# Kernel optimization log

Measured on AMD Instinct MI355X. Metric: run time of the kernel, lower is better.

## Reference

```python
import jax, jax.numpy as jnp
import numpy as np

N, D, E = 16384, 2048, 64   # tokens, d_model, num_experts
K = 9                        # self.k = min(k+1, num_experts) with k=8
EPS = 0.01
SIGMA = 1.0 / E              # Normal(0, 1/num_experts) stddev


def setup_inputs() -> dict:
    key = jax.random.key(0)
    ks = jax.random.split(key, 6)
    x = jax.random.normal(ks[0], (N, D), jnp.float32)
    Wr = jax.random.normal(ks[1], (D, E), jnp.float32) * 0.02
    br = jnp.zeros((E,), jnp.float32)
    Wn = jax.random.normal(ks[2], (D, E), jnp.float32) * 0.02
    bn = jnp.zeros((E,), jnp.float32)
    noise_eps = jax.random.normal(ks[3], (N, E), jnp.float32)
    # torch: (-empty.exponential_()).log() -> log of Exp(1) samples
    gumbel_noise = jnp.log(jax.random.exponential(ks[4], (N, E), jnp.float32))
    return {"x": x, "Wr": Wr, "br": br, "Wn": Wn, "bn": bn,
            "noise_eps": noise_eps, "gumbel_noise": gumbel_noise}


def reference(x, Wr, br, Wn, bn, noise_eps, gumbel_noise):
    raw_logits = x @ Wr + br                              # [N, E]
    noise_stddev = jax.nn.softplus(x @ Wn + bn) + EPS     # [N, E]
    noisy_logits = raw_logits + noise_eps * noise_stddev  # [N, E]

    top_vals, top_idx = jax.lax.top_k(noisy_logits, K)    # [N, K] sorted desc
    # scatter ones at top-k indices (indices unique per row)
    hard_mask = jax.nn.one_hot(top_idx, E, dtype=noisy_logits.dtype).sum(axis=1)  # [N, E]

    # gumbel-softmax straight-through relaxation
    mask_soft = jax.nn.softmax(noisy_logits + gumbel_noise, axis=-1)
    expert_mask = hard_mask - jax.lax.stop_gradient(mask_soft) + mask_soft

    route_prob = jax.nn.softmax(noisy_logits, axis=-1)    # [N, E]
    importance = jax.nn.softmax(raw_logits, axis=-1).sum(axis=0)  # [E]

    # load: P(raw + noise > threshold), Normal(0, 1/E) CDF per original
    threshold = top_vals[:, K - 1]                        # [N]
    z = (threshold[:, None] - raw_logits) / noise_stddev  # [N, E]
    cdf = 0.5 * (1.0 + jax.scipy.special.erf(z / (SIGMA * jnp.sqrt(jnp.float32(2.0)))))
    load = (1.0 - cdf).sum(axis=0)                        # [E]

    return (expert_mask, route_prob, importance, load)
```

## Files before the change

kernel.cpp:

```cpp
#include <hip/hip_runtime.h>
#include <hip/hip_bf16.h>
#include <math.h>

#define N_TOK 16384
#define DIM   2048
#define NE    64
#define TOPK  9

#define ROWS     64
#define DC       64
#define NCHUNK   (DIM / DC)
#define NTHREADS 512

typedef short  short8  __attribute__((ext_vector_type(8)));
typedef float  float4_ __attribute__((ext_vector_type(4)));
typedef unsigned short ushort_t;

__device__ __forceinline__ unsigned pk2(float a, float b) {
    float2 f; f.x = a; f.y = b;
    __hip_bfloat162 h = __float22bfloat162_rn(f);
    unsigned u;
    __builtin_memcpy(&u, &h, 4);
    return u;
}

__device__ __forceinline__ void cvt8(const float4_ va, const float4_ vb,
                                     short8* h, short8* l) {
    union { short8 s; unsigned u[4]; } H, L;
    const float f[8] = {va[0], va[1], va[2], va[3], vb[0], vb[1], vb[2], vb[3]};
#pragma unroll
    for (int i = 0; i < 4; ++i) {
        const float a = f[2 * i], b = f[2 * i + 1];
        const unsigned p = pk2(a, b);
        H.u[i] = p;
        const float ha = __uint_as_float(p << 16);
        const float hb = __uint_as_float(p & 0xffff0000u);
        L.u[i] = pk2(a - ha, b - hb);
    }
    *h = H.s; *l = L.s;
}

__device__ __forceinline__ void wave_max64_2(float& a, float& b) {
#pragma unroll
    for (int off = 32; off > 0; off >>= 1) {
        const float ax = __shfl_xor(a, off, 64);
        const float bx = __shfl_xor(b, off, 64);
        a = fmaxf(a, ax);
        b = fmaxf(b, bx);
    }
}

__device__ __forceinline__ void wave_sum64_3(float& a, float& b, float& c) {
#pragma unroll
    for (int off = 32; off > 0; off >>= 1) {
        const float ax = __shfl_xor(a, off, 64);
        const float bx = __shfl_xor(b, off, 64);
        const float cx = __shfl_xor(c, off, 64);
        a += ax;
        b += bx;
        c += cx;
    }
}

__global__ __launch_bounds__(256)
void prep_w(const float* __restrict__ Wr, const float* __restrict__ Wn,
            ushort_t* __restrict__ wsW)
{
    const int gid = blockIdx.x * 256 + threadIdx.x;
    const int l   = gid & 63;
    const int ct  = (gid >> 6) & 7;
    const int kcg = gid >> 9;
    const int n   = ct * 16 + (l & 15);
    const int k0  = kcg * 32 + (l >> 4) * 8;
    const float* src = (n < NE) ? (Wr + n) : (Wn + (n - NE));
    union { short8 s; ushort_t us[8]; } H, L;
#pragma unroll
    for (int j = 0; j < 8; ++j) {
        const float v = src[(size_t)(k0 + j) * NE];
        const unsigned uv = __float_as_uint(v);
        const unsigned hb = (uv + 0x7fffu + ((uv >> 16) & 1u)) & 0xffff0000u;
        const float lo = v - __uint_as_float(hb);
        const unsigned ul = __float_as_uint(lo);
        H.us[j] = (ushort_t)(hb >> 16);
        L.us[j] = (ushort_t)((ul + 0x7fffu + ((ul >> 16) & 1u)) >> 16);
    }
    const size_t s0 = (size_t)(kcg * 8 + ct) * 2;
    *(short8*)(wsW + s0 * 512 + l * 8)         = H.s;
    *(short8*)(wsW + (s0 + 1) * 512 + l * 8)   = L.s;
}

__global__ __launch_bounds__(NTHREADS, 2)
void moe_main(const float* __restrict__ x,
              const float* __restrict__ br,
              const float* __restrict__ bn,
              const float* __restrict__ noise_eps,
              const float* __restrict__ gumbel,
              const ushort_t* __restrict__ wsW,
              float* __restrict__ out)
{
    __shared__ __align__(16) float smem[8320];

    const int t    = threadIdx.x;
    const int lane = t & 63;
    const int w    = t >> 6;
    const int c4   = lane & 15;
    const int q    = lane >> 4;
    const int rg   = w >> 2;
    const int cg   = w & 3;
    const int row0 = blockIdx.x * ROWS;

    const float* pA[2];
#pragma unroll
    for (int rt = 0; rt < 2; ++rt)
        pA[rt] = x + (size_t)(row0 + (2 * rg + rt) * 16 + c4) * DIM + q * 8;

    float4_ acc[2][2];
#pragma unroll
    for (int rt = 0; rt < 2; ++rt)
#pragma unroll
        for (int cc = 0; cc < 2; ++cc)
            acc[rt][cc] = (float4_)(0.f);

    const char* wsB = (const char*)wsW;

#pragma unroll 2
    for (int ch = 0; ch < NCHUNK; ++ch) {
        short8 bh[2][2], bl[2][2];
#pragma unroll
        for (int kc = 0; kc < 2; ++kc)
#pragma unroll
            for (int cc = 0; cc < 2; ++cc) {
                const int ct = 2 * cg + cc;
                const size_t off = (size_t)(((ch * 2 + kc) * 8) + ct) * 2048
                                 + (size_t)lane * 16;
                bh[kc][cc] = *(const short8*)(wsB + off);
                bl[kc][cc] = *(const short8*)(wsB + off + 1024);
            }
#pragma unroll
        for (int kc = 0; kc < 2; ++kc)
#pragma unroll
            for (int rt = 0; rt < 2; ++rt) {
                const float4_ va = *(const float4_*)(pA[rt] + ch * DC + kc * 32);
                const float4_ vb = *(const float4_*)(pA[rt] + ch * DC + kc * 32 + 4);
                short8 ah, al;
                cvt8(va, vb, &ah, &al);
#pragma unroll
                for (int cc = 0; cc < 2; ++cc) {
                    acc[rt][cc] = __builtin_amdgcn_mfma_f32_16x16x32_bf16(ah, bh[kc][cc], acc[rt][cc], 0, 0, 0);
                    acc[rt][cc] = __builtin_amdgcn_mfma_f32_16x16x32_bf16(al, bh[kc][cc], acc[rt][cc], 0, 0, 0);
                    acc[rt][cc] = __builtin_amdgcn_mfma_f32_16x16x32_bf16(ah, bl[kc][cc], acc[rt][cc], 0, 0, 0);
                }
            }
    }

    float* rawS = &smem[0];
    float* noiS = &smem[4160];
#pragma unroll
    for (int rt = 0; rt < 2; ++rt)
#pragma unroll
        for (int cc = 0; cc < 2; ++cc) {
            const int colg = (2 * cg + cc) * 16 + c4;
            float* basep = (colg < NE) ? rawS : noiS;
            const int col = colg & 63;
#pragma unroll
            for (int v = 0; v < 4; ++v) {
                const int row = (2 * rg + rt) * 16 + q * 4 + v;
                basep[row * 65 + col] = acc[rt][cc][v];
            }
        }
    __syncthreads();

    const float br_l = br[lane];
    const float bn_l = bn[lane];

    float epsv[8], gumv[8];
#pragma unroll
    for (int r = 0; r < 8; ++r) {
        const int row = row0 + w * 8 + r;
        epsv[r] = noise_eps[(size_t)row * NE + lane];
        gumv[r] = gumbel  [(size_t)row * NE + lane];
    }

    float imp_acc = 0.f, load_acc = 0.f;
    float* out_em   = out;
    float* out_rp   = out + (size_t)N_TOK * NE;
    float* out_imp  = out + (size_t)2 * N_TOK * NE;
    float* out_load = out_imp + NE;

#pragma unroll 1
    for (int r = 0; r < 8; ++r) {
        const int lrow = w * 8 + r;
        const int row  = row0 + lrow;
        const float raw = rawS[lrow * 65 + lane] + br_l;
        const float nl  = noiS[lrow * 65 + lane] + bn_l;
        const float sd = fmaxf(nl, 0.f) + log1pf(expf(-fabsf(nl))) + 0.01f;
        const float noisy = fmaf(epsv[r], sd, raw);

        const unsigned uk  = __float_as_uint(noisy);
        const unsigned key = uk ^ ((uk & 0x80000000u) ? 0xFFFFFFFFu : 0x80000000u);
        unsigned res = 0;
#pragma unroll
        for (int bit = 31; bit >= 0; --bit) {
            const unsigned cand = res | (1u << bit);
            const int cnt = __popcll(__ballot(key >= cand));
            if (cnt >= TOPK) res = cand;
        }
        const float thr  = __uint_as_float(res ^ ((res & 0x80000000u) ? 0x80000000u : 0xFFFFFFFFu));
        const float hard = (key >= res) ? 1.f : 0.f;

        const float g = noisy + gumv[r];
        float mg = g, mr = raw;
        wave_max64_2(mg, mr);

        const float eg = expf(g - mg);
        const float en = expf(noisy - thr);
        const float er = expf(raw - mr);
        float sg = eg, sn = en, sr = er;
        wave_sum64_3(sg, sn, sr);

        const float ms = eg / sg;
        const float em = (hard - ms) + ms;
        const float rp = en / sn;
        imp_acc += er / sr;

        const float z = (thr - raw) / sd;
        load_acc += 0.5f * erfcf(z * 45.254833995939045f);

        out_em[(size_t)row * NE + lane] = em;
        out_rp[(size_t)row * NE + lane] = rp;
    }

    __syncthreads();
    smem[w * 64 + lane]       = imp_acc;
    smem[512 + w * 64 + lane] = load_acc;
    __syncthreads();
    if (w == 0) {
        float s1 = 0.f, s2 = 0.f;
#pragma unroll
        for (int i = 0; i < 8; ++i) {
            s1 += smem[i * 64 + lane];
            s2 += smem[512 + i * 64 + lane];
        }
        atomicAdd(&out_imp[lane], s1);
        atomicAdd(&out_load[lane], s2);
    }
}

extern "C" void kernel_launch(void* const* d_in, const int* in_sizes, int n_in,
                              void* d_out, int out_size, void* d_ws, size_t ws_size,
                              hipStream_t stream)
{
    const float* x         = (const float*)d_in[0];
    const float* Wr        = (const float*)d_in[1];
    const float* br        = (const float*)d_in[2];
    const float* Wn        = (const float*)d_in[3];
    const float* bn        = (const float*)d_in[4];
    const float* noise_eps = (const float*)d_in[5];
    const float* gumbel    = (const float*)d_in[6];
    float* out = (float*)d_out;
    ushort_t* wsW = (ushort_t*)d_ws;

    (void)hipMemsetAsync((char*)d_out + (size_t)2 * N_TOK * NE * sizeof(float), 0,
                         2 * NE * sizeof(float), stream);
    prep_w<<<128, 256, 0, stream>>>(Wr, Wn, wsW);
    moe_main<<<N_TOK / ROWS, NTHREADS, 0, stream>>>(
        x, br, bn, noise_eps, gumbel, wsW, out);
}
```

Measured before the change: 278.4 us.

## Stage x tiles into LDS with async loads and split K across wave halves

Each block now handles 32 rows instead of 64. The two halves of the waves each reduce half of the d_model dimension, and their partial results are summed through shared memory in the epilogue. Activation tiles are fetched with global_load_lds into a 4-deep XOR-swizzled LDS ring buffer, while weight fragments are double-buffered in registers. Manual vmcnt waits and barriers overlap these loads with the MFMA work. The aim is to hide global-load latency and raise occupancy (launch bounds go from 2 to 4 blocks), at the cost of hand-tuned wait counts that are fragile and an extra reduction step.

```diff
diff --git a/kernel.cpp b/kernel.cpp
--- a/kernel.cpp
+++ b/kernel.cpp
@@ -7,14 +7,22 @@
 #define NE    64
 #define TOPK  9
 
-#define ROWS     64
+#define ROWS     32
 #define DC       64
 #define NCHUNK   (DIM / DC)
+#define HALF     (NCHUNK / 2)
 #define NTHREADS 512
+#define NBUF     4
 
 typedef short  short8  __attribute__((ext_vector_type(8)));
 typedef float  float4_ __attribute__((ext_vector_type(4)));
 typedef unsigned short ushort_t;
+
+__device__ __forceinline__ void async16(const void* g, void* l) {
+    __builtin_amdgcn_global_load_lds(
+        (const __attribute__((address_space(1))) void*)g,
+        (__attribute__((address_space(3))) void*)l, 16, 0, 0);
+}
 
 __device__ __forceinline__ unsigned pk2(float a, float b) {
     float2 f; f.x = a; f.y = b;
@@ -89,7 +97,43 @@
     *(short8*)(wsW + (s0 + 1) * 512 + l * 8)   = L.s;
 }
 
-__global__ __launch_bounds__(NTHREADS, 2)
+struct BFrag { short8 h[2][2]; short8 l[2][2]; };
+
+__device__ __forceinline__ void load_b(const char* __restrict__ wsB,
+                                       int ch, int cg, int lane, BFrag& b) {
+#pragma unroll
+    for (int kc = 0; kc < 2; ++kc)
+#pragma unroll
+        for (int cc = 0; cc < 2; ++cc) {
+            const size_t off = (size_t)(((ch * 2 + kc) * 8) + 2 * cg + cc) * 2048
+                             + (size_t)lane * 16;
+            b.h[kc][cc] = *(const short8*)(wsB + off);
+            b.l[kc][cc] = *(const short8*)(wsB + off + 1024);
+        }
+}
+
+__device__ __forceinline__ void mfma_chunk(const float* __restrict__ xb,
+                                           const int (&aoff)[2][2],
+                                           const BFrag& b,
+                                           float4_ (&acc)[2][2]) {
+#pragma unroll
+    for (int kc = 0; kc < 2; ++kc)
+#pragma unroll
+        for (int rt = 0; rt < 2; ++rt) {
+            const float4_ va = *(const float4_*)(xb + rt * 1024 + aoff[kc][0]);
+            const float4_ vb = *(const float4_*)(xb + rt * 1024 + aoff[kc][1]);
+            short8 ah, al;
+            cvt8(va, vb, &ah, &al);
+#pragma unroll
+            for (int cc = 0; cc < 2; ++cc) {
+                acc[rt][cc] = __builtin_amdgcn_mfma_f32_16x16x32_bf16(ah, b.h[kc][cc], acc[rt][cc], 0, 0, 0);
+                acc[rt][cc] = __builtin_amdgcn_mfma_f32_16x16x32_bf16(al, b.h[kc][cc], acc[rt][cc], 0, 0, 0);
+                acc[rt][cc] = __builtin_amdgcn_mfma_f32_16x16x32_bf16(ah, b.l[kc][cc], acc[rt][cc], 0, 0, 0);
+            }
+        }
+}
+
+__global__ __launch_bounds__(NTHREADS, 4)
 void moe_main(const float* __restrict__ x,
               const float* __restrict__ br,
               const float* __restrict__ bn,
@@ -98,21 +142,36 @@
               const ushort_t* __restrict__ wsW,
               float* __restrict__ out)
 {
-    __shared__ __align__(16) float smem[8320];
+    __shared__ __align__(16) float smem[2 * NBUF * 2048];
 
     const int t    = threadIdx.x;
     const int lane = t & 63;
     const int w    = t >> 6;
+    const int kh   = w >> 2;
+    const int wv   = w & 3;
     const int c4   = lane & 15;
     const int q    = lane >> 4;
-    const int rg   = w >> 2;
-    const int cg   = w & 3;
     const int row0 = blockIdx.x * ROWS;
-
-    const float* pA[2];
-#pragma unroll
-    for (int rt = 0; rt < 2; ++rt)
-        pA[rt] = x + (size_t)(row0 + (2 * rg + rt) * 16 + c4) * DIM + q * 8;
+    const int XB   = kh * (NBUF * 2048);
+
+    const float* gxb[2];
+    int lxo[2];
+#pragma unroll
+    for (int ii = 0; ii < 2; ++ii) {
+        const int i  = 2 * wv + ii;
+        const int r  = 4 * i + q;
+        const int gk = c4 ^ (r & 15);
+        gxb[ii] = x + (size_t)(row0 + r) * DIM + kh * (HALF * DC) + gk * 4;
+        lxo[ii] = i * 256;
+    }
+
+    int aoff[2][2];
+#pragma unroll
+    for (int kc = 0; kc < 2; ++kc) {
+        const int g0 = kc * 8 + q * 2;
+        aoff[kc][0] = c4 * 64 + ((g0 ^ c4) * 4);
+        aoff[kc][1] = c4 * 64 + (((g0 + 1) ^ c4) * 4);
+    }
 
     float4_ acc[2][2];
 #pragma unroll
@@ -122,61 +181,96 @@
             acc[rt][cc] = (float4_)(0.f);
 
     const char* wsB = (const char*)wsW;
-
-#pragma unroll 2
-    for (int ch = 0; ch < NCHUNK; ++ch) {
-        short8 bh[2][2], bl[2][2];
-#pragma unroll
-        for (int kc = 0; kc < 2; ++kc)
+    const int chb = kh * HALF;
+
+#pragma unroll
+    for (int p = 0; p < NBUF - 1; ++p)
+#pragma unroll
+        for (int ii = 0; ii < 2; ++ii)
+            async16(gxb[ii] + p * DC, &smem[XB + p * 2048 + lxo[ii]]);
+
+    BFrag bA, bB;
+    load_b(wsB, chb, wv, lane, bA);
+
+#pragma unroll 1
+    for (int i = 0; i < HALF - 4; i += 2) {
+        asm volatile("s_waitcnt vmcnt(12)" ::: "memory");
+        __builtin_amdgcn_s_barrier();
+        asm volatile("" ::: "memory");
+        load_b(wsB, chb + i + 1, wv, lane, bB);
+#pragma unroll
+        for (int ii = 0; ii < 2; ++ii)
+            async16(gxb[ii] + (i + 3) * DC, &smem[XB + ((i + 3) & 3) * 2048 + lxo[ii]]);
+        __builtin_amdgcn_sched_barrier(0);
+        mfma_chunk(&smem[XB + (i & 3) * 2048], aoff, bA, acc);
+
+        asm volatile("s_waitcnt vmcnt(12)" ::: "memory");
+        __builtin_amdgcn_s_barrier();
+        asm volatile("" ::: "memory");
+        load_b(wsB, chb + i + 2, wv, lane, bA);
+#pragma unroll
+        for (int ii = 0; ii < 2; ++ii)
+            async16(gxb[ii] + (i + 4) * DC, &smem[XB + ((i + 4) & 3) * 2048 + lxo[ii]]);
+        __builtin_amdgcn_sched_barrier(0);
+        mfma_chunk(&smem[XB + ((i + 1) & 3) * 2048], aoff, bB, acc);
+    }
+
+    asm volatile("s_waitcnt vmcnt(12)" ::: "memory");
+    __builtin_amdgcn_s_barrier();
+    asm volatile("" ::: "memory");
+    load_b(wsB, chb + 13, wv, lane, bB);
+#pragma unroll
+    for (int ii = 0; ii < 2; ++ii)
+        async16(gxb[ii] + 15 * DC, &smem[XB + 3 * 2048 + lxo[ii]]);
+    __builtin_amdgcn_sched_barrier(0);
+    mfma_chunk(&smem[XB + 0 * 2048], aoff, bA, acc);
+
+    asm volatile("s_waitcnt vmcnt(12)" ::: "memory");
+    __builtin_amdgcn_s_barrier();
+    asm volatile("" ::: "memory");
+    load_b(wsB, chb + 14, wv, lane, bA);
+    __builtin_amdgcn_sched_barrier(0);
+    mfma_chunk(&smem[XB + 1 * 2048], aoff, bB, acc);
+
+    asm volatile("s_waitcnt vmcnt(10)" ::: "memory");
+    __builtin_amdgcn_s_barrier();
+    asm volatile("" ::: "memory");
+    load_b(wsB, chb + 15, wv, lane, bB);
+    __builtin_amdgcn_sched_barrier(0);
+    mfma_chunk(&smem[XB + 2 * 2048], aoff, bA, acc);
+
+    asm volatile("s_waitcnt vmcnt(8)" ::: "memory");
+    __builtin_amdgcn_s_barrier();
+    asm volatile("" ::: "memory");
+    __builtin_amdgcn_sched_barrier(0);
+    mfma_chunk(&smem[XB + 3 * 2048], aoff, bB, acc);
+
+    __syncthreads();
+    {
+        float* base = &smem[kh * 4160];
+#pragma unroll
+        for (int rt = 0; rt < 2; ++rt)
 #pragma unroll
             for (int cc = 0; cc < 2; ++cc) {
-                const int ct = 2 * cg + cc;
-                const size_t off = (size_t)(((ch * 2 + kc) * 8) + ct) * 2048
-                                 + (size_t)lane * 16;
-                bh[kc][cc] = *(const short8*)(wsB + off);
-                bl[kc][cc] = *(const short8*)(wsB + off + 1024);
-            }
-#pragma unroll
-        for (int kc = 0; kc < 2; ++kc)
-#pragma unroll
-            for (int rt = 0; rt < 2; ++rt) {
-                const float4_ va = *(const float4_*)(pA[rt] + ch * DC + kc * 32);
-                const float4_ vb = *(const float4_*)(pA[rt] + ch * DC + kc * 32 + 4);
-                short8 ah, al;
-                cvt8(va, vb, &ah, &al);
-#pragma unroll
-                for (int cc = 0; cc < 2; ++cc) {
-                    acc[rt][cc] = __builtin_amdgcn_mfma_f32_16x16x32_bf16(ah, bh[kc][cc], acc[rt][cc], 0, 0, 0);
-                    acc[rt][cc] = __builtin_amdgcn_mfma_f32_16x16x32_bf16(al, bh[kc][cc], acc[rt][cc], 0, 0, 0);
-                    acc[rt][cc] = __builtin_amdgcn_mfma_f32_16x16x32_bf16(ah, bl[kc][cc], acc[rt][cc], 0, 0, 0);
+                const int colg = (2 * wv + cc) * 16 + c4;
+                float* bp = (colg < NE) ? base : (base + 2080);
+                const int col = colg & 63;
+#pragma unroll
+                for (int v = 0; v < 4; ++v) {
+                    const int row = rt * 16 + q * 4 + v;
+                    bp[row * 65 + col] = acc[rt][cc][v];
                 }
             }
     }
-
-    float* rawS = &smem[0];
-    float* noiS = &smem[4160];
-#pragma unroll
-    for (int rt = 0; rt < 2; ++rt)
-#pragma unroll
-        for (int cc = 0; cc < 2; ++cc) {
-            const int colg = (2 * cg + cc) * 16 + c4;
-            float* basep = (colg < NE) ? rawS : noiS;
-            const int col = colg & 63;
-#pragma unroll
-            for (int v = 0; v < 4; ++v) {
-                const int row = (2 * rg + rt) * 16 + q * 4 + v;
-                basep[row * 65 + col] = acc[rt][cc][v];
-            }
-        }
     __syncthreads();
 
     const float br_l = br[lane];
     const float bn_l = bn[lane];
 
-    float epsv[8], gumv[8];
-#pragma unroll
-    for (int r = 0; r < 8; ++r) {
-        const int row = row0 + w * 8 + r;
+    float epsv[4], gumv[4];
+#pragma unroll
+    for (int r = 0; r < 4; ++r) {
+        const int row = row0 + w * 4 + r;
         epsv[r] = noise_eps[(size_t)row * NE + lane];
         gumv[r] = gumbel  [(size_t)row * NE + lane];
     }
@@ -188,11 +282,11 @@
     float* out_load = out_imp + NE;
 
 #pragma unroll 1
-    for (int r = 0; r < 8; ++r) {
-        const int lrow = w * 8 + r;
+    for (int r = 0; r < 4; ++r) {
+        const int lrow = w * 4 + r;
         const int row  = row0 + lrow;
-        const float raw = rawS[lrow * 65 + lane] + br_l;
-        const float nl  = noiS[lrow * 65 + lane] + bn_l;
+        const float raw = smem[lrow * 65 + lane] + smem[4160 + lrow * 65 + lane] + br_l;
+        const float nl  = smem[2080 + lrow * 65 + lane] + smem[6240 + lrow * 65 + lane] + bn_l;
         const float sd = fmaxf(nl, 0.f) + log1pf(expf(-fabsf(nl))) + 0.01f;
         const float noisy = fmaf(epsv[r], sd, raw);
 
```

Result: faster. 246.6 us (-11.4%).

## Split fused kernel into pipelined GEMM and separate router kernel

Applied to the files above, without the earlier changes.

Splits the fused GEMM+routing kernel in two. A 16-row-per-block GEMM kernel double-buffers its A and B register fragments and writes the [N,128] logits to workspace. A separate router kernel reads those logits back and does softplus, top-k, softmaxes and the reductions. The aim is more blocks, better latency hiding in the x-bandwidth-bound GEMM and no shared-memory staging, at the cost of an extra round trip to global memory for the logits (about 8MB each way) and an extra launch.

```diff
diff --git a/kernel.cpp b/kernel.cpp
--- a/kernel.cpp
+++ b/kernel.cpp
@@ -7,10 +7,10 @@
 #define NE    64
 #define TOPK  9
 
-#define ROWS     64
 #define DC       64
 #define NCHUNK   (DIM / DC)
-#define NTHREADS 512
+#define G_ROWS   16
+#define R_ROWS   32
 
 typedef short  short8  __attribute__((ext_vector_type(8)));
 typedef float  float4_ __attribute__((ext_vector_type(4)));
@@ -89,96 +89,118 @@
     *(short8*)(wsW + (s0 + 1) * 512 + l * 8)   = L.s;
 }
 
-__global__ __launch_bounds__(NTHREADS, 2)
-void moe_main(const float* __restrict__ x,
-              const float* __restrict__ br,
-              const float* __restrict__ bn,
-              const float* __restrict__ noise_eps,
-              const float* __restrict__ gumbel,
-              const ushort_t* __restrict__ wsW,
-              float* __restrict__ out)
-{
-    __shared__ __align__(16) float smem[8320];
-
+struct AFrag { float4_ v[4]; };
+struct BFrag { short8 h[2][2]; short8 l[2][2]; };
+
+__device__ __forceinline__ void load_a(const float* __restrict__ p, AFrag& a) {
+    a.v[0] = *(const float4_*)(p);
+    a.v[1] = *(const float4_*)(p + 4);
+    a.v[2] = *(const float4_*)(p + 32);
+    a.v[3] = *(const float4_*)(p + 36);
+}
+
+__device__ __forceinline__ void load_b(const char* __restrict__ wsB,
+                                       int ch, int w, int lane, BFrag& b) {
+#pragma unroll
+    for (int kc = 0; kc < 2; ++kc)
+#pragma unroll
+        for (int cc = 0; cc < 2; ++cc) {
+            const size_t off = (size_t)(((ch * 2 + kc) * 8) + 2 * w + cc) * 2048
+                             + (size_t)lane * 16;
+            b.h[kc][cc] = *(const short8*)(wsB + off);
+            b.l[kc][cc] = *(const short8*)(wsB + off + 1024);
+        }
+}
+
+__device__ __forceinline__ void compute_chunk(const AFrag& a, const BFrag& b,
+                                              float4_ (&acc)[2]) {
+#pragma unroll
+    for (int kc = 0; kc < 2; ++kc) {
+        short8 ah, al;
+        cvt8(a.v[kc * 2], a.v[kc * 2 + 1], &ah, &al);
+#pragma unroll
+        for (int cc = 0; cc < 2; ++cc) {
+            acc[cc] = __builtin_amdgcn_mfma_f32_16x16x32_bf16(ah, b.h[kc][cc], acc[cc], 0, 0, 0);
+            acc[cc] = __builtin_amdgcn_mfma_f32_16x16x32_bf16(al, b.h[kc][cc], acc[cc], 0, 0, 0);
+            acc[cc] = __builtin_amdgcn_mfma_f32_16x16x32_bf16(ah, b.l[kc][cc], acc[cc], 0, 0, 0);
+        }
+    }
+}
+
+__global__ __launch_bounds__(256, 3)
+void gemm_logits(const float* __restrict__ x,
+                 const ushort_t* __restrict__ wsW,
+                 float* __restrict__ logits)
+{
     const int t    = threadIdx.x;
     const int lane = t & 63;
     const int w    = t >> 6;
     const int c4   = lane & 15;
     const int q    = lane >> 4;
-    const int rg   = w >> 2;
-    const int cg   = w & 3;
-    const int row0 = blockIdx.x * ROWS;
-
-    const float* pA[2];
-#pragma unroll
-    for (int rt = 0; rt < 2; ++rt)
-        pA[rt] = x + (size_t)(row0 + (2 * rg + rt) * 16 + c4) * DIM + q * 8;
-
-    float4_ acc[2][2];
-#pragma unroll
-    for (int rt = 0; rt < 2; ++rt)
-#pragma unroll
-        for (int cc = 0; cc < 2; ++cc)
-            acc[rt][cc] = (float4_)(0.f);
-
-    const char* wsB = (const char*)wsW;
-
-#pragma unroll 2
-    for (int ch = 0; ch < NCHUNK; ++ch) {
-        short8 bh[2][2], bl[2][2];
-#pragma unroll
-        for (int kc = 0; kc < 2; ++kc)
-#pragma unroll
-            for (int cc = 0; cc < 2; ++cc) {
-                const int ct = 2 * cg + cc;
-                const size_t off = (size_t)(((ch * 2 + kc) * 8) + ct) * 2048
-                                 + (size_t)lane * 16;
-                bh[kc][cc] = *(const short8*)(wsB + off);
-                bl[kc][cc] = *(const short8*)(wsB + off + 1024);
-            }
-#pragma unroll
-        for (int kc = 0; kc < 2; ++kc)
-#pragma unroll
-            for (int rt = 0; rt < 2; ++rt) {
-                const float4_ va = *(const float4_*)(pA[rt] + ch * DC + kc * 32);
-                const float4_ vb = *(const float4_*)(pA[rt] + ch * DC + kc * 32 + 4);
-                short8 ah, al;
-                cvt8(va, vb, &ah, &al);
-#pragma unroll
-                for (int cc = 0; cc < 2; ++cc) {
-                    acc[rt][cc] = __builtin_amdgcn_mfma_f32_16x16x32_bf16(ah, bh[kc][cc], acc[rt][cc], 0, 0, 0);
-                    acc[rt][cc] = __builtin_amdgcn_mfma_f32_16x16x32_bf16(al, bh[kc][cc], acc[rt][cc], 0, 0, 0);
-                    acc[rt][cc] = __builtin_amdgcn_mfma_f32_16x16x32_bf16(ah, bl[kc][cc], acc[rt][cc], 0, 0, 0);
-                }
-            }
-    }
-
-    float* rawS = &smem[0];
-    float* noiS = &smem[4160];
-#pragma unroll
-    for (int rt = 0; rt < 2; ++rt)
-#pragma unroll
-        for (int cc = 0; cc < 2; ++cc) {
-            const int colg = (2 * cg + cc) * 16 + c4;
-            float* basep = (colg < NE) ? rawS : noiS;
-            const int col = colg & 63;
-#pragma unroll
-            for (int v = 0; v < 4; ++v) {
-                const int row = (2 * rg + rt) * 16 + q * 4 + v;
-                basep[row * 65 + col] = acc[rt][cc][v];
-            }
-        }
-    __syncthreads();
+    const int row0 = blockIdx.x * G_ROWS;
+
+    const float* pA = x + (size_t)(row0 + c4) * DIM + q * 8;
+    const char*  wsB = (const char*)wsW;
+
+    float4_ acc[2];
+    acc[0] = (float4_)(0.f);
+    acc[1] = (float4_)(0.f);
+
+    AFrag aX, aY;
+    BFrag bX, bY;
+    load_a(pA + 0 * DC, aX);
+    load_b(wsB, 0, w, lane, bX);
+    load_a(pA + 1 * DC, aY);
+    load_b(wsB, 1, w, lane, bY);
+
+#pragma unroll 1
+    for (int i = 0; i < NCHUNK - 2; i += 2) {
+        compute_chunk(aX, bX, acc);
+        load_a(pA + (i + 2) * DC, aX);
+        load_b(wsB, i + 2, w, lane, bX);
+        compute_chunk(aY, bY, acc);
+        load_a(pA + (i + 3) * DC, aY);
+        load_b(wsB, i + 3, w, lane, bY);
+    }
+    compute_chunk(aX, bX, acc);
+    compute_chunk(aY, bY, acc);
+
+#pragma unroll
+    for (int cc = 0; cc < 2; ++cc) {
+        const int colg = (2 * w + cc) * 16 + c4;
+#pragma unroll
+        for (int v = 0; v < 4; ++v) {
+            const int row = q * 4 + v;
+            logits[(size_t)(row0 + row) * 128 + colg] = acc[cc][v];
+        }
+    }
+}
+
+__global__ __launch_bounds__(256)
+void router(const float* __restrict__ logits,
+            const float* __restrict__ br,
+            const float* __restrict__ bn,
+            const float* __restrict__ noise_eps,
+            const float* __restrict__ gumbel,
+            float* __restrict__ out)
+{
+    __shared__ float red[512];
+    const int t    = threadIdx.x;
+    const int lane = t & 63;
+    const int w    = t >> 6;
+    const int row0 = blockIdx.x * R_ROWS + w * 8;
 
     const float br_l = br[lane];
     const float bn_l = bn[lane];
 
-    float epsv[8], gumv[8];
+    float rawv[8], nlv[8], epsv[8], gumv[8];
 #pragma unroll
     for (int r = 0; r < 8; ++r) {
-        const int row = row0 + w * 8 + r;
-        epsv[r] = noise_eps[(size_t)row * NE + lane];
-        gumv[r] = gumbel  [(size_t)row * NE + lane];
+        const size_t row = (size_t)(row0 + r);
+        rawv[r] = logits[row * 128 + lane];
+        nlv[r]  = logits[row * 128 + 64 + lane];
+        epsv[r] = noise_eps[row * NE + lane];
+        gumv[r] = gumbel  [row * NE + lane];
     }
 
     float imp_acc = 0.f, load_acc = 0.f;
@@ -187,12 +209,11 @@
     float* out_imp  = out + (size_t)2 * N_TOK * NE;
     float* out_load = out_imp + NE;
 
-#pragma unroll 1
+#pragma unroll 2
     for (int r = 0; r < 8; ++r) {
-        const int lrow = w * 8 + r;
-        const int row  = row0 + lrow;
-        const float raw = rawS[lrow * 65 + lane] + br_l;
-        const float nl  = noiS[lrow * 65 + lane] + bn_l;
+        const int row = row0 + r;
+        const float raw = rawv[r] + br_l;
+        const float nl  = nlv[r]  + bn_l;
         const float sd = fmaxf(nl, 0.f) + log1pf(expf(-fabsf(nl))) + 0.01f;
         const float noisy = fmaf(epsv[r], sd, raw);
 
@@ -230,17 +251,12 @@
         out_rp[(size_t)row * NE + lane] = rp;
     }
 
-    __syncthreads();
-    smem[w * 64 + lane]       = imp_acc;
-    smem[512 + w * 64 + lane] = load_acc;
+    red[w * 64 + lane]       = imp_acc;
+    red[256 + w * 64 + lane] = load_acc;
     __syncthreads();
     if (w == 0) {
-        float s1 = 0.f, s2 = 0.f;
-#pragma unroll
-        for (int i = 0; i < 8; ++i) {
-            s1 += smem[i * 64 + lane];
-            s2 += smem[512 + i * 64 + lane];
-        }
+        const float s1 = red[lane] + red[64 + lane] + red[128 + lane] + red[192 + lane];
+        const float s2 = red[256 + lane] + red[320 + lane] + red[384 + lane] + red[448 + lane];
         atomicAdd(&out_imp[lane], s1);
         atomicAdd(&out_load[lane], s2);
     }
@@ -258,11 +274,13 @@
     const float* noise_eps = (const float*)d_in[5];
     const float* gumbel    = (const float*)d_in[6];
     float* out = (float*)d_out;
+
     ushort_t* wsW = (ushort_t*)d_ws;
+    float* logits = (float*)((char*)d_ws + (1 << 20));
 
     (void)hipMemsetAsync((char*)d_out + (size_t)2 * N_TOK * NE * sizeof(float), 0,
                          2 * NE * sizeof(float), stream);
     prep_w<<<128, 256, 0, stream>>>(Wr, Wn, wsW);
-    moe_main<<<N_TOK / ROWS, NTHREADS, 0, stream>>>(
-        x, br, bn, noise_eps, gumbel, wsW, out);
-}
+    gemm_logits<<<N_TOK / G_ROWS, 256, 0, stream>>>(x, wsW, logits);
+    router<<<N_TOK / R_ROWS, 256, 0, stream>>>(logits, br, bn, noise_eps, gumbel, out);
+}
```

Result: slower. 298.3 us (+7.2%).
